# Kernel optimization log

Measured on AMD Instinct MI355X. Metric: run time of the kernel, lower is better.

Reference implementation:

```python
import jax, jax.numpy as jnp
import numpy as np

B, S, DIM, H = 2, 2048, 1024, 16
DH = DIM // H            # 64
G = DH // 4              # 16 quaternion groups per head
IQ = DIM // 4            # 256
ROPE_BASE = 10000.0
SCALE = DH ** -0.5


def qlinear(x, wr, wi, wj, wk, b):
    # x: [B,S,4*IQ]; strided quaternion components, exact combo from QuaternionLinear.forward
    xr, xi, xj, xk = x[..., 0::4], x[..., 1::4], x[..., 2::4], x[..., 3::4]
    o_r = xr @ wr.T - xi @ wi.T - xj @ wj.T - xk @ wk.T
    o_i = xi @ wr.T + xr @ wi.T + xk @ wk.T - xj @ wj.T
    o_j = xj @ wr.T - xk @ wk.T + xr @ wj.T + xi @ wi.T
    o_k = xk @ wr.T + xj @ wj.T - xi @ wi.T + xr @ wk.T
    out = jnp.stack([o_r, o_i, o_j, o_k], axis=-1).reshape(x.shape[:-1] + (-1,))
    return out + b


def qrope(x):
    # x: [B,H,S,DH]; left quaternion multiply u(theta) \otimes q, axis_mode='cycle'
    b, h, s, dh = x.shape
    g = dh // 4
    xq = x.reshape(b, h, s, g, 4)
    t = jnp.arange(s, dtype=x.dtype)
    inv = 1.0 / (ROPE_BASE ** (jnp.arange(g, dtype=x.dtype) / g))
    ang = t[:, None] * inv[None, :]            # [S,G]
    cos, sin = jnp.cos(ang), jnp.sin(ang)
    gi = jnp.arange(g)
    ax_i = (gi % 3 == 0).astype(x.dtype)
    ax_j = (gi % 3 == 1).astype(x.dtype)
    ax_k = (gi % 3 == 2).astype(x.dtype)
    ur, ui, uj, uk = cos, sin * ax_i, sin * ax_j, sin * ax_k   # [S,G] broadcast over [B,H,S,G]
    xr, xi, xj, xk = xq[..., 0], xq[..., 1], xq[..., 2], xq[..., 3]
    pr = ur * xr - ui * xi - uj * xj - uk * xk
    pi = ur * xi + ui * xr + uj * xk - uk * xj
    pj = ur * xj - ui * xk + uj * xr + uk * xi
    pk = ur * xk + ui * xj - uj * xi + uk * xr
    return jnp.stack([pr, pi, pj, pk], axis=-1).reshape(b, h, s, dh)


def setup_inputs() -> dict:
    key = jax.random.key(0)
    ks = jax.random.split(key, 24)
    x = jax.random.normal(ks[0], (B, S, DIM), dtype=jnp.float32)
    # causal mask: True = masked
    mask = jnp.broadcast_to(jnp.triu(jnp.ones((S, S), dtype=bool), k=1), (B, S, S))
    inp = {"x": x, "mask": mask}
    i = 1
    for proj in ("q", "k", "v", "o"):
        for comp in ("wr", "wi", "wj", "wk"):
            inp[f"{proj}_{comp}"] = jax.random.normal(ks[i], (IQ, IQ), dtype=jnp.float32) * 0.02
            i += 1
        inp[f"{proj}_b"] = jnp.zeros((DIM,), dtype=jnp.float32)
    return inp


def reference(x, mask,
              q_wr, q_wi, q_wj, q_wk, q_b,
              k_wr, k_wi, k_wj, k_wk, k_b,
              v_wr, v_wi, v_wj, v_wk, v_b,
              o_wr, o_wi, o_wj, o_wk, o_b):
    b, s, dm = x.shape
    q = qlinear(x, q_wr, q_wi, q_wj, q_wk, q_b).reshape(b, s, H, DH).transpose(0, 2, 1, 3)
    k = qlinear(x, k_wr, k_wi, k_wj, k_wk, k_b).reshape(b, s, H, DH).transpose(0, 2, 1, 3)
    v = qlinear(x, v_wr, v_wi, v_wj, v_wk, v_b).reshape(b, s, H, DH).transpose(0, 2, 1, 3)
    q, k = qrope(q), qrope(k)
    scores = jnp.einsum('bhsd,bhtd->bhst', q, k) * SCALE
    scores = jnp.where(mask[:, None, :, :], -jnp.inf, scores)
    a = jax.nn.softmax(scores, axis=-1)
    out = jnp.einsum('bhst,bhtd->bhsd', a, v).transpose(0, 2, 1, 3).reshape(b, s, dm)
    return qlinear(out, o_wr, o_wi, o_wj, o_wk, o_b)
```

## Files before the change

### kernel.cpp

```cpp
#include <hip/hip_runtime.h>
#include <stdint.h>

typedef unsigned short u16;
typedef unsigned int   u32;

#define NB   2
#define NS   2048
#define NDIM 1024
#define NH   16
#define NDH  64
#define QSCALE 0.18033688011112042f

typedef __bf16 bf16x8 __attribute__((ext_vector_type(8)));
typedef float  f32x4  __attribute__((ext_vector_type(4)));

#define MFMA_BF16(a,b,c) __builtin_amdgcn_mfma_f32_16x16x32_bf16((a),(b),(c),0,0,0)

#define XBF_OFF   (256)
#define WD_OFF    (XBF_OFF  + 8*1024*1024)
#define BIAS_OFF  (WD_OFF   + 8*1024*1024)
#define QB_OFF    (BIAS_OFF + 16384)
#define KB_OFF    (QB_OFF   + 8*1024*1024)
#define VT_OFF    (KB_OFF   + 8*1024*1024)
#define OP_OFF    (VT_OFF   + 8*1024*1024)
#define LP_OFF    (OP_OFF   + 16*1024*1024)

__device__ __forceinline__ float bf2f(u16 h){
  union { u32 u; float f; } v; v.u = ((u32)h) << 16; return v.f;
}
__device__ __forceinline__ u16 f2bf(float f){
  union { float f; u32 u; } v; v.f = f;
  u32 r = (v.u >> 16) & 1u;
  return (u16)((v.u + 0x7fffu + r) >> 16);
}
__device__ __forceinline__ u16 f2bf_rn(float f){
  union { __bf16 h; u16 u; } v; v.h = (__bf16)f; return v.u;
}
__device__ __forceinline__ float load_val(const void* p, int i, int isbf){
  return isbf ? bf2f(((const u16*)p)[i]) : ((const float*)p)[i];
}
__device__ __forceinline__ void gl_lds16(const u16* g, u16* l){
  __builtin_amdgcn_global_load_lds(
      (__attribute__((address_space(1))) void*)(uintptr_t)g,
      (__attribute__((address_space(3))) void*)(uintptr_t)l,
      16, 0, 0);
}

struct QPtrs { const void* w[16]; const void* b[4]; };

__global__ void prep_kernel(const void* __restrict__ xin, QPtrs ptrs,
                            u16* __restrict__ xbf, u16* __restrict__ wd,
                            float* __restrict__ biasf, int* __restrict__ flag){
  __shared__ int cnt;
  if (threadIdx.x == 0) cnt = 0;
  __syncthreads();
  {
    const uint4* xv = (const uint4*)xin;
    uint4 v0 = xv[threadIdx.x * 2], v1 = xv[threadIdx.x * 2 + 1];
    const u16* hh = (const u16*)&v0;
    int ok = 0;
#pragma unroll
    for (int i = 0; i < 16; ++i){
      u16 h = (i < 8) ? hh[i] : ((const u16*)&v1)[i - 8];
      int e = (h >> 7) & 0xFF;
      if ((e > 96 && e < 158) || ((h & 0x7FFF) == 0)) ok++;
    }
    atomicAdd(&cnt, ok);
  }
  __syncthreads();
  int isbf = (cnt > 3600) ? 1 : 0;
  if (blockIdx.x == 0 && threadIdx.x == 0) *flag = isbf;

  int idx = blockIdx.x * 256 + threadIdx.x;

  if (blockIdx.x < 2048){
    int t = idx;
    if (isbf){
      ((uint4*)xbf)[t] = ((const uint4*)xin)[t];
    } else {
      const float4* f4 = (const float4*)xin;
      float4 a = f4[2*t], b = f4[2*t+1];
      ushort4 lo = { f2bf(a.x), f2bf(a.y), f2bf(a.z), f2bf(a.w) };
      ushort4 hi = { f2bf(b.x), f2bf(b.y), f2bf(b.z), f2bf(b.w) };
      ((ushort4*)xbf)[2*t]   = lo;
      ((ushort4*)xbf)[2*t+1] = hi;
    }
  } else {
    int wi = idx - 2048 * 256;
    int n = wi & 255, m = (wi >> 8) & 255, p = wi >> 16;
    int src = m * 256 + n;
    float vr = load_val(ptrs.w[p*4+0], src, isbf);
    float vi = load_val(ptrs.w[p*4+1], src, isbf);
    float vj = load_val(ptrs.w[p*4+2], src, isbf);
    float vk = load_val(ptrs.w[p*4+3], src, isbf);
    ushort4 s0 = { f2bf(vr), f2bf(-vi), f2bf(-vj), f2bf(-vk) };
    ushort4 s1 = { f2bf(vi), f2bf(vr),  f2bf(-vj), f2bf(vk)  };
    ushort4 s2 = { f2bf(vj), f2bf(vi),  f2bf(vr),  f2bf(-vk) };
    ushort4 s3 = { f2bf(vk), f2bf(-vi), f2bf(vj),  f2bf(vr)  };
    u16* base = &wd[(size_t)p * 1048576 + (size_t)(4*m) * 1024 + 4*n];
    *(ushort4*)(base)        = s0;
    *(ushort4*)(base + 1024) = s1;
    *(ushort4*)(base + 2048) = s2;
    *(ushort4*)(base + 3072) = s3;
    if (wi < 4096){
      int pp = wi >> 10, oo = wi & 1023;
      biasf[wi] = load_val(ptrs.b[pp], oo, isbf);
    }
  }
}

__global__ __launch_bounds__(256)
void gemm_qkv_kernel(const u16* __restrict__ A, const u16* __restrict__ Bw,
                     const float* __restrict__ bias,
                     u16* __restrict__ qb, u16* __restrict__ kb, u16* __restrict__ vt){
  __shared__ u16 sA[3][128 * 32];
  __shared__ u16 sB[3][128 * 32];
  int tid = threadIdx.x, w = tid >> 6, lane = tid & 63, quad = lane >> 4, l16 = lane & 15;

  int lid = (int)blockIdx.y * 24 + (int)blockIdx.x;
  int swz = (lid & 7) * 96 + (lid >> 3);
  int n0 = (swz % 24) * 128, m0 = (swz / 24) * 128;

  f32x4 acc[4][4];
#pragma unroll
  for (int i = 0; i < 4; ++i)
#pragma unroll
    for (int j = 0; j < 4; ++j) acc[i][j] = (f32x4){0.f, 0.f, 0.f, 0.f};

  int cp = lane & 3, rl = lane >> 2;
  int gc = (cp ^ ((rl >> 1) & 3)) * 8;
  const u16* ga = A  + (size_t)(m0 + w*16 + rl) * 1024 + gc;
  const u16* gb = Bw + (size_t)(n0 + w*16 + rl) * 1024 + gc;
  int ldo = w * 512 + lane * 8;
  int xorv = ((l16 >> 1) & 3) * 8;
  int mw = (w & 1) * 64, nw = (w >> 1) * 64;

  auto stage = [&](int k0, int b){
#pragma unroll
    for (int i = 0; i < 2; ++i){
      gl_lds16(ga + (size_t)i * 65536 + k0, &sA[b][ldo + i * 2048]);
      gl_lds16(gb + (size_t)i * 65536 + k0, &sB[b][ldo + i * 2048]);
    }
  };

  stage(0, 0);
  stage(32, 1);
  asm volatile("s_waitcnt vmcnt(4)" ::: "memory");
  __builtin_amdgcn_s_barrier();

  int bcur = 0, bnxt = 2;
  for (int it = 0; it < 32; ++it){
    if (it < 30) stage((it + 2) * 32, bnxt);
    const u16* cA = sA[bcur];
    const u16* cB = sB[bcur];
    bf16x8 af[4], bfr[4];
#pragma unroll
    for (int mt = 0; mt < 4; ++mt)
      af[mt] = *(const bf16x8*)&cA[(mw + mt*16 + l16) * 32 + (quad*8 ^ xorv)];
#pragma unroll
    for (int nt = 0; nt < 4; ++nt)
      bfr[nt] = *(const bf16x8*)&cB[(nw + nt*16 + l16) * 32 + (quad*8 ^ xorv)];
#pragma unroll
    for (int mt = 0; mt < 4; ++mt)
#pragma unroll
      for (int nt = 0; nt < 4; ++nt)
        acc[mt][nt] = MFMA_BF16(af[mt], bfr[nt], acc[mt][nt]);

    if (it < 30) asm volatile("s_waitcnt vmcnt(4)" ::: "memory");
    else         asm volatile("s_waitcnt vmcnt(0)" ::: "memory");
    __builtin_amdgcn_s_barrier();
    bcur = (bcur == 2) ? 0 : bcur + 1;
    bnxt = (bnxt == 2) ? 0 : bnxt + 1;
  }

  int proj = n0 >> 10;
  if (proj == 2){
#pragma unroll
    for (int mt = 0; mt < 4; ++mt){
      int row = m0 + mw + mt*16 + quad*4;
      int b = row >> 11, seq0 = row & 2047;
#pragma unroll
      for (int nt = 0; nt < 4; ++nt){
        int col = n0 + nw + nt*16 + l16;
        int o = col & 1023, h = o >> 6, d = o & 63;
        float bv = bias[col];
        ushort4 pv = { f2bf_rn(acc[mt][nt][0] + bv), f2bf_rn(acc[mt][nt][1] + bv),
                       f2bf_rn(acc[mt][nt][2] + bv), f2bf_rn(acc[mt][nt][3] + bv) };
        *(ushort4*)&vt[((size_t)((b*16 + h) * 64 + d)) * 2048 + seq0] = pv;
      }
    }
  } else {
    float sc = (proj == 0) ? QSCALE : 1.0f;
    u16* dst = proj ? kb : qb;
    int c = l16 & 3;
#pragma unroll
    for (int nt = 0; nt < 4; ++nt){
      int col = n0 + nw + nt*16 + l16;
      int o = col & 1023, h = o >> 6, d = o & 63;
      int g = d >> 2;
      int ax = g % 3;
      int mask = ax + 1;
      int tbl = (ax == 0) ? 0xA : (ax == 1 ? 0x6 : 0xC);
      float sgn = ((tbl >> c) & 1) ? 1.f : -1.f;
      float inv = __builtin_amdgcn_exp2f(-(float)g * 0.8304820237218405f);
      float bv = bias[col];
#pragma unroll
      for (int mt = 0; mt < 4; ++mt){
        int row0 = m0 + mw + mt*16 + quad*4;
        int b = row0 >> 11, s0 = row0 & 2047;
        size_t obase = ((size_t)((b*16 + h) * 2048 + s0)) * 64 + d;
#pragma unroll
        for (int r = 0; r < 4; ++r){
          float v = acc[mt][nt][r] + bv;
          float vp = __shfl_xor(v, mask);
          float ang = (float)(s0 + r) * inv;
          float co = __cosf(ang) * sc;
          float si = __sinf(ang) * sc * sgn;
          dst[obase + (size_t)r * 64] = f2bf_rn(co * v + si * vp);
        }
      }
    }
  }
}

__global__ __launch_bounds__(256)
void gemm_o_kernel(const u16* __restrict__ A, const u16* __restrict__ Bw,
                   const float* __restrict__ bias, void* __restrict__ dout,
                   const int* __restrict__ flag){
  __shared__ u16 sA[3][64 * 32];
  __shared__ u16 sB[3][128 * 32];
  int tid = threadIdx.x, w = tid >> 6, lane = tid & 63, quad = lane >> 4, l16 = lane & 15;
  int n0 = blockIdx.x * 128, m0 = blockIdx.y * 64;

  f32x4 acc[2][4];
#pragma unroll
  for (int i = 0; i < 2; ++i)
#pragma unroll
    for (int j = 0; j < 4; ++j) acc[i][j] = (f32x4){0.f, 0.f, 0.f, 0.f};

  int cp = lane & 3, rl = lane >> 2;
  int gc = (cp ^ ((rl >> 1) & 3)) * 8;
  int xorv = ((l16 >> 1) & 3) * 8;
  int mw = (w & 1) * 32, nw = (w >> 1) * 64;

  auto stage = [&](int k0, int b){
#pragma unroll
    for (int i = 0; i < 3; ++i){
      int ch = w * 3 + i;
      int lr = (ch < 4 ? ch : ch - 4) * 16 + rl;
      int eo = (ch < 4 ? ch : ch - 4) * 512 + lane * 8;
      if (ch < 4) gl_lds16(A  + (size_t)(m0 + lr) * 1024 + k0 + gc, &sA[b][eo]);
      else        gl_lds16(Bw + (size_t)(n0 + lr) * 1024 + k0 + gc, &sB[b][eo]);
    }
  };

  stage(0, 0);
  stage(32, 1);
  asm volatile("s_waitcnt vmcnt(3)" ::: "memory");
  __builtin_amdgcn_s_barrier();

  int bcur = 0, bnxt = 2;
  for (int it = 0; it < 32; ++it){
    if (it < 30) stage((it + 2) * 32, bnxt);
    const u16* cA = sA[bcur];
    const u16* cB = sB[bcur];
    bf16x8 af[2], bfr[4];
#pragma unroll
    for (int mt = 0; mt < 2; ++mt)
      af[mt] = *(const bf16x8*)&cA[(mw + mt*16 + l16) * 32 + (quad*8 ^ xorv)];
#pragma unroll
    for (int nt = 0; nt < 4; ++nt)
      bfr[nt] = *(const bf16x8*)&cB[(nw + nt*16 + l16) * 32 + (quad*8 ^ xorv)];
#pragma unroll
    for (int mt = 0; mt < 2; ++mt)
#pragma unroll
      for (int nt = 0; nt < 4; ++nt)
        acc[mt][nt] = MFMA_BF16(af[mt], bfr[nt], acc[mt][nt]);

    if (it < 30) asm volatile("s_waitcnt vmcnt(3)" ::: "memory");
    else         asm volatile("s_waitcnt vmcnt(0)" ::: "memory");
    __builtin_amdgcn_s_barrier();
    bcur = (bcur == 2) ? 0 : bcur + 1;
    bnxt = (bnxt == 2) ? 0 : bnxt + 1;
  }

  int isbf = *flag;
#pragma unroll
  for (int mt = 0; mt < 2; ++mt){
    int row = m0 + mw + mt*16 + quad*4;
#pragma unroll
    for (int nt = 0; nt < 4; ++nt){
      int col = n0 + nw + nt*16 + l16;
      float bv = bias[col];
#pragma unroll
      for (int r = 0; r < 4; ++r){
        float val = acc[mt][nt][r] + bv;
        size_t addr = (size_t)(row + r) * 1024 + col;
        if (isbf) ((u16*)dout)[addr] = f2bf(val);
        else      ((float*)dout)[addr] = val;
      }
    }
  }
}

#define SPT 20

__global__ __launch_bounds__(128, 2)
void attn_kernel(const u16* __restrict__ Q, const u16* __restrict__ K,
                 const u16* __restrict__ Vt, u16* __restrict__ OP,
                 float* __restrict__ LP){
  __shared__ u16 sK[2][4096];
  __shared__ u16 sPT[2][2][64 * SPT];
  int lid = (int)blockIdx.x + 32 * (int)blockIdx.y + 64 * (int)blockIdx.z;
  int bh  = (lid & 7) * 4 + ((lid >> 3) & 3);
  int spl = (lid >> 5) & 1;
  int z   = lid >> 6;
  int tid = threadIdx.x, w = tid >> 6, lane = tid & 63, quad = lane >> 4, l16 = lane & 15;
  size_t kbase = (size_t)bh * 2048 * 64;
  size_t vbase = (size_t)bh * 64 * 2048;

  auto stage = [&](int kt, int b){
    int kcol = kt * 64;
#pragma unroll
    for (int p = 0; p < 4; ++p){
      int sb = (w*4 + p) * 64;
      int slot = sb + lane;
      int row = slot >> 3, dc = (slot & 7) ^ (row & 7);
      gl_lds16(K + kbase + (size_t)(kcol + row) * 64 + dc*8, &sK[b][sb * 8]);
    }
  };

  for (int item = 0; item < 2; ++item){
    int s2 = item ? z : 31 - z;
    int rowbase = s2 * 64 + w * 32;

    bf16x8 qf[2][2];
#pragma unroll
    for (int g = 0; g < 2; ++g)
#pragma unroll
      for (int kc = 0; kc < 2; ++kc)
        qf[g][kc] = *(const bf16x8*)(Q + kbase + (size_t)(rowbase + g*16 + l16) * 64 + kc*32 + quad*8);

    f32x4 oaccT[2][4];
    float lsum[2][4];
#pragma unroll
    for (int g = 0; g < 2; ++g)
#pragma unroll
      for (int i = 0; i < 4; ++i){ oaccT[g][i] = (f32x4){0.f,0.f,0.f,0.f}; lsum[g][i] = 0.f; }

    int c = (s2 + 2) >> 1;
    int kt0 = spl ? c : 0;
    int ntiles = spl ? (s2 + 1 - c) : c;

    stage(kt0, 0);
    for (int i = 0; i < ntiles; ++i){
      int kcol = (kt0 + i) * 64;
      __syncthreads();
      if (i + 1 < ntiles) stage(kt0 + i + 1, (i + 1) & 1);
      const u16* bK = sK[i & 1];

      if (kcol <= rowbase + 31){
        bf16x8 vf[4][2];
#pragma unroll
        for (int dn = 0; dn < 4; ++dn)
#pragma unroll
          for (int kc = 0; kc < 2; ++kc)
            vf[dn][kc] = *(const bf16x8*)(Vt + vbase + (size_t)(dn*16 + l16) * 2048
                                          + kcol + kc*32 + quad*8);
        bf16x8 bk[2][4];
#pragma unroll
        for (int kc = 0; kc < 2; ++kc)
#pragma unroll
          for (int nt = 0; nt < 4; ++nt){
            int rw = nt*16 + l16;
            int ch = ((kc*4 + quad) ^ (rw & 7)) * 8;
            bk[kc][nt] = *(const bf16x8*)&bK[rw*64 + ch];
          }
#pragma unroll
        for (int g = 0; g < 2; ++g){
          int G0 = rowbase + g*16;
          if (kcol <= G0 + 15){
            u16* spg = &sPT[w][g][0];
            f32x4 sacc[4];
#pragma unroll
            for (int nt = 0; nt < 4; ++nt) sacc[nt] = (f32x4){0.f,0.f,0.f,0.f};
#pragma unroll
            for (int kc = 0; kc < 2; ++kc)
#pragma unroll
              for (int nt = 0; nt < 4; ++nt)
                sacc[nt] = MFMA_BF16(qf[g][kc], bk[kc][nt], sacc[nt]);

            if (kcol + 63 > G0){
#pragma unroll
              for (int nt = 0; nt < 4; ++nt){
                int col = kcol + nt*16 + l16;
                ushort4 pv;
#pragma unroll
                for (int r = 0; r < 4; ++r){
                  int row = G0 + quad*4 + r;
                  float pp = (col <= row) ? __builtin_amdgcn_exp2f(sacc[nt][r]) : 0.f;
                  lsum[g][r] += pp;
                  ((u16*)&pv)[r] = f2bf_rn(pp);
                }
                *(ushort4*)&spg[(nt*16 + l16) * SPT + quad*4] = pv;
              }
            } else {
#pragma unroll
              for (int nt = 0; nt < 4; ++nt){
                ushort4 pv;
#pragma unroll
                for (int r = 0; r < 4; ++r){
                  float pp = __builtin_amdgcn_exp2f(sacc[nt][r]);
                  lsum[g][r] += pp;
                  ((u16*)&pv)[r] = f2bf_rn(pp);
                }
                *(ushort4*)&spg[(nt*16 + l16) * SPT + quad*4] = pv;
              }
            }
#pragma unroll
            for (int kc = 0; kc < 2; ++kc){
              bf16x8 pf;
#pragma unroll
              for (int j = 0; j < 8; ++j)
                pf[j] = ((const __bf16*)spg)[(kc*32 + quad*8 + j) * SPT + l16];
#pragma unroll
              for (int dn = 0; dn < 4; ++dn)
                oaccT[g][dn] = MFMA_BF16(vf[dn][kc], pf, oaccT[g][dn]);
            }
          }
        }
      }
    }

    float* scr = (float*)&sPT[w][0][0];
#pragma unroll
    for (int g = 0; g < 2; ++g)
#pragma unroll
      for (int r = 0; r < 4; ++r){
        float l = lsum[g][r];
        l += __shfl_xor(l, 1); l += __shfl_xor(l, 2);
        l += __shfl_xor(l, 4); l += __shfl_xor(l, 8);
        if (l16 == 0) scr[g*16 + quad*4 + r] = l;
      }
    float lrow[2];
#pragma unroll
    for (int g = 0; g < 2; ++g) lrow[g] = scr[g*16 + l16];

    size_t obase = ((size_t)(spl*32 + bh)) * 2048;
#pragma unroll
    for (int g = 0; g < 2; ++g){
      int row = rowbase + g*16 + l16;
      if (quad == 0) LP[obase + row] = lrow[g];
#pragma unroll
      for (int dn = 0; dn < 4; ++dn){
        ushort4 ov = { f2bf_rn(oaccT[g][dn][0]), f2bf_rn(oaccT[g][dn][1]),
                       f2bf_rn(oaccT[g][dn][2]), f2bf_rn(oaccT[g][dn][3]) };
        *(ushort4*)&OP[(obase + row) * 64 + dn*16 + quad*4] = ov;
      }
    }

    __syncthreads();
  }
}

__global__ void combine_kernel(const u16* __restrict__ OP, const float* __restrict__ LP,
                               u16* __restrict__ Ab){
  int idx = blockIdx.x * 256 + threadIdx.x;
  int dc = idx & 7, s = (idx >> 3) & 2047, bh = idx >> 14;
  size_t r0 = (size_t)bh * 2048 + s, r1 = (size_t)(32 + bh) * 2048 + s;
  float invl = 1.f / (LP[r0] + LP[r1]);
  union { uint4 v; u16 h[8]; } a0, a1, o;
  a0.v = *(const uint4*)&OP[r0 * 64 + dc*8];
  a1.v = *(const uint4*)&OP[r1 * 64 + dc*8];
#pragma unroll
  for (int j = 0; j < 8; ++j)
    o.h[j] = f2bf((bf2f(a0.h[j]) + bf2f(a1.h[j])) * invl);
  int b = bh >> 4, h = bh & 15;
  *(uint4*)&Ab[((size_t)(b*2048 + s)) * 1024 + h*64 + dc*8] = o.v;
}

extern "C" void kernel_launch(void* const* d_in, const int* in_sizes, int n_in,
                              void* d_out, int out_size, void* d_ws, size_t ws_size,
                              hipStream_t stream){
  (void)in_sizes; (void)n_in; (void)out_size; (void)ws_size;
  char* ws = (char*)d_ws;
  int*   flag  = (int*)ws;
  u16*   Xbf   = (u16*)(ws + XBF_OFF);
  u16*   Wd    = (u16*)(ws + WD_OFF);
  float* biasf = (float*)(ws + BIAS_OFF);
  u16*   Qb    = (u16*)(ws + QB_OFF);
  u16*   Kb    = (u16*)(ws + KB_OFF);
  u16*   Vt    = (u16*)(ws + VT_OFF);
  u16*   OP    = (u16*)(ws + OP_OFF);
  float* LP    = (float*)(ws + LP_OFF);
  u16*   Ab    = Xbf;

  QPtrs ptrs;
  for (int p = 0; p < 4; ++p){
    for (int wi = 0; wi < 4; ++wi) ptrs.w[p*4 + wi] = d_in[2 + p*5 + wi];
    ptrs.b[p] = d_in[2 + p*5 + 4];
  }

  prep_kernel<<<3072, 256, 0, stream>>>(d_in[0], ptrs, Xbf, Wd, biasf, flag);
  gemm_qkv_kernel<<<dim3(24, 32), 256, 0, stream>>>(Xbf, Wd, biasf, Qb, Kb, Vt);
  attn_kernel<<<dim3(32, 2, 16), 128, 0, stream>>>(Qb, Kb, Vt, OP, LP);
  combine_kernel<<<2048, 256, 0, stream>>>(OP, LP, Ab);
  gemm_o_kernel<<<dim3(8, 64), 256, 0, stream>>>(Ab, Wd + 3*1048576, biasf + 3072,
                                                 d_out, flag);
}
```

Baseline: 240.0 us.

## Halve attention query tile to 32 rows per block and double grid

The attention kernel now gives each block 32 query rows (16 per wave) instead of 64, and launches twice as many blocks, with causal pairing over 64 row-blocks. The goal is more parallelism and finer load balance across CUs, and fewer registers per wave from dropping the second 16-row group. In exchange each staged K tile and each V fragment load is reused by half as many query rows, so global and LDS traffic per FLOP roughly doubles. Splits where ntiles is zero are now guarded.

```diff
diff --git a/kernel.cpp b/kernel.cpp
--- a/kernel.cpp
+++ b/kernel.cpp
@@ -310,7 +310,7 @@
                  const u16* __restrict__ Vt, u16* __restrict__ OP,
                  float* __restrict__ LP){
   __shared__ u16 sK[2][4096];
-  __shared__ u16 sPT[2][2][64 * SPT];
+  __shared__ u16 sPT[2][64 * SPT];
   int lid = (int)blockIdx.x + 32 * (int)blockIdx.y + 64 * (int)blockIdx.z;
   int bh  = (lid & 7) * 4 + ((lid >> 3) & 3);
   int spl = (lid >> 5) & 1;
@@ -318,6 +318,7 @@
   int tid = threadIdx.x, w = tid >> 6, lane = tid & 63, quad = lane >> 4, l16 = lane & 15;
   size_t kbase = (size_t)bh * 2048 * 64;
   size_t vbase = (size_t)bh * 64 * 2048;
+  u16* spw = &sPT[w][0];
 
   auto stage = [&](int kt, int b){
     int kcol = kt * 64;
@@ -331,35 +332,32 @@
   };
 
   for (int item = 0; item < 2; ++item){
-    int s2 = item ? z : 31 - z;
-    int rowbase = s2 * 64 + w * 32;
-
-    bf16x8 qf[2][2];
-#pragma unroll
-    for (int g = 0; g < 2; ++g)
-#pragma unroll
-      for (int kc = 0; kc < 2; ++kc)
-        qf[g][kc] = *(const bf16x8*)(Q + kbase + (size_t)(rowbase + g*16 + l16) * 64 + kc*32 + quad*8);
-
-    f32x4 oaccT[2][4];
-    float lsum[2][4];
-#pragma unroll
-    for (int g = 0; g < 2; ++g)
-#pragma unroll
-      for (int i = 0; i < 4; ++i){ oaccT[g][i] = (f32x4){0.f,0.f,0.f,0.f}; lsum[g][i] = 0.f; }
-
-    int c = (s2 + 2) >> 1;
+    int s2 = item ? z : 63 - z;
+    int rowbase = s2 * 32 + w * 16;
+
+    bf16x8 qf[2];
+#pragma unroll
+    for (int kc = 0; kc < 2; ++kc)
+      qf[kc] = *(const bf16x8*)(Q + kbase + (size_t)(rowbase + l16) * 64 + kc*32 + quad*8);
+
+    f32x4 oaccT[4];
+    float lsum[4];
+#pragma unroll
+    for (int i = 0; i < 4; ++i){ oaccT[i] = (f32x4){0.f,0.f,0.f,0.f}; lsum[i] = 0.f; }
+
+    int ntot = (s2 >> 1) + 1;
+    int c = (ntot + 1) >> 1;
     int kt0 = spl ? c : 0;
-    int ntiles = spl ? (s2 + 1 - c) : c;
-
-    stage(kt0, 0);
+    int ntiles = spl ? (ntot - c) : c;
+
+    if (ntiles > 0) stage(kt0, 0);
     for (int i = 0; i < ntiles; ++i){
       int kcol = (kt0 + i) * 64;
       __syncthreads();
       if (i + 1 < ntiles) stage(kt0 + i + 1, (i + 1) & 1);
       const u16* bK = sK[i & 1];
 
-      if (kcol <= rowbase + 31){
+      if (kcol <= rowbase + 15){
         bf16x8 vf[4][2];
 #pragma unroll
         for (int dn = 0; dn < 4; ++dn)
@@ -376,85 +374,74 @@
             int ch = ((kc*4 + quad) ^ (rw & 7)) * 8;
             bk[kc][nt] = *(const bf16x8*)&bK[rw*64 + ch];
           }
-#pragma unroll
-        for (int g = 0; g < 2; ++g){
-          int G0 = rowbase + g*16;
-          if (kcol <= G0 + 15){
-            u16* spg = &sPT[w][g][0];
-            f32x4 sacc[4];
-#pragma unroll
-            for (int nt = 0; nt < 4; ++nt) sacc[nt] = (f32x4){0.f,0.f,0.f,0.f};
-#pragma unroll
-            for (int kc = 0; kc < 2; ++kc)
-#pragma unroll
-              for (int nt = 0; nt < 4; ++nt)
-                sacc[nt] = MFMA_BF16(qf[g][kc], bk[kc][nt], sacc[nt]);
-
-            if (kcol + 63 > G0){
-#pragma unroll
-              for (int nt = 0; nt < 4; ++nt){
-                int col = kcol + nt*16 + l16;
-                ushort4 pv;
-#pragma unroll
-                for (int r = 0; r < 4; ++r){
-                  int row = G0 + quad*4 + r;
-                  float pp = (col <= row) ? __builtin_amdgcn_exp2f(sacc[nt][r]) : 0.f;
-                  lsum[g][r] += pp;
-                  ((u16*)&pv)[r] = f2bf_rn(pp);
-                }
-                *(ushort4*)&spg[(nt*16 + l16) * SPT + quad*4] = pv;
-              }
-            } else {
-#pragma unroll
-              for (int nt = 0; nt < 4; ++nt){
-                ushort4 pv;
-#pragma unroll
-                for (int r = 0; r < 4; ++r){
-                  float pp = __builtin_amdgcn_exp2f(sacc[nt][r]);
-                  lsum[g][r] += pp;
-                  ((u16*)&pv)[r] = f2bf_rn(pp);
-                }
-                *(ushort4*)&spg[(nt*16 + l16) * SPT + quad*4] = pv;
-              }
+        int G0 = rowbase;
+        f32x4 sacc[4];
+#pragma unroll
+        for (int nt = 0; nt < 4; ++nt) sacc[nt] = (f32x4){0.f,0.f,0.f,0.f};
+#pragma unroll
+        for (int kc = 0; kc < 2; ++kc)
+#pragma unroll
+          for (int nt = 0; nt < 4; ++nt)
+            sacc[nt] = MFMA_BF16(qf[kc], bk[kc][nt], sacc[nt]);
+
+        if (kcol + 63 > G0){
+#pragma unroll
+          for (int nt = 0; nt < 4; ++nt){
+            int col = kcol + nt*16 + l16;
+            ushort4 pv;
+#pragma unroll
+            for (int r = 0; r < 4; ++r){
+              int row = G0 + quad*4 + r;
+              float pp = (col <= row) ? __builtin_amdgcn_exp2f(sacc[nt][r]) : 0.f;
+              lsum[r] += pp;
+              ((u16*)&pv)[r] = f2bf_rn(pp);
             }
-#pragma unroll
-            for (int kc = 0; kc < 2; ++kc){
-              bf16x8 pf;
-#pragma unroll
-              for (int j = 0; j < 8; ++j)
-                pf[j] = ((const __bf16*)spg)[(kc*32 + quad*8 + j) * SPT + l16];
-#pragma unroll
-              for (int dn = 0; dn < 4; ++dn)
-                oaccT[g][dn] = MFMA_BF16(vf[dn][kc], pf, oaccT[g][dn]);
+            *(ushort4*)&spw[(nt*16 + l16) * SPT + quad*4] = pv;
+          }
+        } else {
+#pragma unroll
+          for (int nt = 0; nt < 4; ++nt){
+            ushort4 pv;
+#pragma unroll
+            for (int r = 0; r < 4; ++r){
+              float pp = __builtin_amdgcn_exp2f(sacc[nt][r]);
+              lsum[r] += pp;
+              ((u16*)&pv)[r] = f2bf_rn(pp);
             }
+            *(ushort4*)&spw[(nt*16 + l16) * SPT + quad*4] = pv;
           }
         }
+#pragma unroll
+        for (int kc = 0; kc < 2; ++kc){
+          bf16x8 pf;
+#pragma unroll
+          for (int j = 0; j < 8; ++j)
+            pf[j] = ((const __bf16*)spw)[(kc*32 + quad*8 + j) * SPT + l16];
+#pragma unroll
+          for (int dn = 0; dn < 4; ++dn)
+            oaccT[dn] = MFMA_BF16(vf[dn][kc], pf, oaccT[dn]);
+        }
       }
     }
 
-    float* scr = (float*)&sPT[w][0][0];
-#pragma unroll
-    for (int g = 0; g < 2; ++g)
-#pragma unroll
-      for (int r = 0; r < 4; ++r){
-        float l = lsum[g][r];
-        l += __shfl_xor(l, 1); l += __shfl_xor(l, 2);
-        l += __shfl_xor(l, 4); l += __shfl_xor(l, 8);
-        if (l16 == 0) scr[g*16 + quad*4 + r] = l;
-      }
-    float lrow[2];
-#pragma unroll
-    for (int g = 0; g < 2; ++g) lrow[g] = scr[g*16 + l16];
+    float* scr = (float*)spw;
+#pragma unroll
+    for (int r = 0; r < 4; ++r){
+      float l = lsum[r];
+      l += __shfl_xor(l, 1); l += __shfl_xor(l, 2);
+      l += __shfl_xor(l, 4); l += __shfl_xor(l, 8);
+      if (l16 == 0) scr[quad*4 + r] = l;
+    }
+    float lrow = scr[l16];
 
     size_t obase = ((size_t)(spl*32 + bh)) * 2048;
-#pragma unroll
-    for (int g = 0; g < 2; ++g){
-      int row = rowbase + g*16 + l16;
-      if (quad == 0) LP[obase + row] = lrow[g];
+    {
+      int row = rowbase + l16;
+      if (quad == 0) LP[obase + row] = lrow;
 #pragma unroll
       for (int dn = 0; dn < 4; ++dn){
-        ushort4 ov = { f2bf_rn(oaccT[g][dn][0]), f2bf_rn(oaccT[g][dn][1]),
-                       f2bf_rn(oaccT[g][dn][2]), f2bf_rn(oaccT[g][dn][3]) };
+        ushort4 ov = { f2bf_rn(oaccT[dn][0]), f2bf_rn(oaccT[dn][1]),
+                       f2bf_rn(oaccT[dn][2]), f2bf_rn(oaccT[dn][3]) };
         *(ushort4*)&OP[(obase + row) * 64 + dn*16 + quad*4] = ov;
       }
     }
@@ -503,7 +490,7 @@
 
   prep_kernel<<<3072, 256, 0, stream>>>(d_in[0], ptrs, Xbf, Wd, biasf, flag);
   gemm_qkv_kernel<<<dim3(24, 32), 256, 0, stream>>>(Xbf, Wd, biasf, Qb, Kb, Vt);
-  attn_kernel<<<dim3(32, 2, 16), 128, 0, stream>>>(Qb, Kb, Vt, OP, LP);
+  attn_kernel<<<dim3(32, 2, 32), 128, 0, stream>>>(Qb, Kb, Vt, OP, LP);
   combine_kernel<<<2048, 256, 0, stream>>>(OP, LP, Ab);
   gemm_o_kernel<<<dim3(8, 64), 256, 0, stream>>>(Ab, Wd + 3*1048576, biasf + 3072,
                                                  d_out, flag);
```

Result: slower. 279.7 us (+16.5%).
